# Performance work log

Measured on AMD Instinct MI355X. Metric: run time of the kernel, lower is better.

Reference implementation:

```python
import jax, jax.numpy as jnp
import numpy as np

DIM = 128
N_HEADS = 4
HEAD_DIM = DIM // N_HEADS  # 32
RANK = 8
SCALING = 16.0 / RANK      # alpha / rank = 2.0
ROPE_BASE = 10000.0
INV_SQRT_HD = 1.0 / float(np.sqrt(HEAD_DIM))


def _rope(x, cos, sin):
    # x: [B, S, H, D]; interleaved-pair rotation matching torch view(..., -1, 2)
    B, S, H, D = x.shape
    xr = x.reshape(B, S, H, D // 2, 2)
    x1, x2 = xr[..., 0], xr[..., 1]
    c = cos[None, :, None, :]  # [1, S, 1, D/2]
    s = sin[None, :, None, :]
    out = jnp.stack([x1 * c - x2 * s, x1 * s + x2 * c], axis=-1)
    return out.reshape(B, S, H, D)


def setup_inputs() -> dict:
    key = jax.random.key(0)
    ks = jax.random.split(key, 11)
    B, S = 128, 256
    w = lambda k, shp: jax.random.normal(k, shp, dtype=jnp.float32) * 0.05
    return {
        "x": jax.random.normal(ks[0], (B, S, DIM), dtype=jnp.float32),
        "wq": w(ks[1], (DIM, DIM)),
        "wk": w(ks[2], (DIM, DIM)),
        "wv": w(ks[3], (DIM, DIM)),
        "wo": w(ks[4], (DIM, DIM)),
        "lora_A_q": w(ks[5], (RANK, DIM)),
        "lora_B_q": w(ks[6], (DIM, RANK)),
        "lora_A_k": w(ks[7], (RANK, DIM)),
        "lora_B_k": w(ks[8], (DIM, RANK)),
        "lora_A_v": w(ks[9], (RANK, DIM)),
        "lora_B_v": w(ks[10], (DIM, RANK)),
    }


def reference(x, wq, wk, wv, wo, lora_A_q, lora_B_q, lora_A_k, lora_B_k,
              lora_A_v, lora_B_v):
    B, S, _ = x.shape
    # RoPE tables (HEAD_DIM split into pairs)
    pos = jnp.arange(S, dtype=jnp.float32)
    inv_freq = 1.0 / (ROPE_BASE ** (jnp.arange(0, HEAD_DIM, 2, dtype=jnp.float32) / HEAD_DIM))
    freqs = pos[:, None] * inv_freq[None, :]  # [S, HEAD_DIM/2]
    cos, sin = jnp.cos(freqs), jnp.sin(freqs)

    def proj(w, A, Bm):
        # base linear (no bias) + LoRA low-rank delta (dropout = eval identity)
        return x @ w.T + (x @ A.T @ Bm.T) * SCALING

    q = proj(wq, lora_A_q, lora_B_q).reshape(B, S, N_HEADS, HEAD_DIM)
    k = proj(wk, lora_A_k, lora_B_k).reshape(B, S, N_HEADS, HEAD_DIM)
    v = proj(wv, lora_A_v, lora_B_v).reshape(B, S, N_HEADS, HEAD_DIM)

    q = _rope(q, cos, sin).transpose(0, 2, 1, 3)  # [B, H, S, D]
    k = _rope(k, cos, sin).transpose(0, 2, 1, 3)
    v = v.transpose(0, 2, 1, 3)

    scores = jnp.einsum('bhqd,bhkd->bhqk', q, k) * INV_SQRT_HD
    causal = jnp.triu(jnp.ones((S, S), dtype=bool), k=1)
    scores = jnp.where(causal[None, None], -jnp.inf, scores)
    attn = jax.nn.softmax(scores, axis=-1)

    out = jnp.einsum('bhqk,bhkd->bhqd', attn, v)
    out = out.transpose(0, 2, 1, 3).reshape(B, S, DIM)
    return out @ wo.T
```

## Files before the change

### kernel.cpp

```cpp
#include <hip/hip_runtime.h>
#include <math.h>

typedef __attribute__((ext_vector_type(8))) short short8;
typedef __attribute__((ext_vector_type(4))) float floatx4;

#define NH 4
#define HD 32
#define DIM 128
#define SEQ 256
#define BATCH 128
#define BS (BATCH*SEQ)
#define RANK 8
#define SCALING 2.0f
#define INV_SQRT_HD 0.17677669529663687f
#define LOG2E 1.4426950408889634f

#if __has_builtin(__builtin_amdgcn_exp2f)
#define EXP2F __builtin_amdgcn_exp2f
#else
#define EXP2F exp2f
#endif

#define QB_OFF  (0ull)
#define KB_OFF  (8ull<<20)
#define VT_OFF  (16ull<<20)
#define XB_OFF  (24ull<<20)
#define WE_OFF  (32ull<<20)
#define TAB_OFF (33ull<<20)

static __device__ __forceinline__ unsigned short f2bf(float f) {
    unsigned u = __float_as_uint(f);
    return (unsigned short)((u + 0x7FFFu + ((u >> 16) & 1u)) >> 16);
}
static __device__ __forceinline__ unsigned packbf(float lo, float hi) {
    unsigned ua = __float_as_uint(lo), ub = __float_as_uint(hi);
    ua += 0x7FFFu + ((ua >> 16) & 1u);
    ub += 0x7FFFu + ((ub >> 16) & 1u);
    return __builtin_amdgcn_perm(ub, ua, 0x07060302);
}

__global__ __launch_bounds__(256) void prep_kernel(
    const float* __restrict__ x,
    const float* __restrict__ wq, const float* __restrict__ wk,
    const float* __restrict__ wv, const float* __restrict__ wo,
    const float* __restrict__ Aq, const float* __restrict__ Bq,
    const float* __restrict__ Ak, const float* __restrict__ Bk,
    const float* __restrict__ Av, const float* __restrict__ Bv,
    unsigned short* __restrict__ weffL, float* __restrict__ tab,
    unsigned short* __restrict__ xbL)
{
    const int bid = blockIdx.x, tid = threadIdx.x;
    if (bid < 32) {
        int t = bid * 256 + tid;
        int m    = t >> 11;
        int kc   = (t >> 9) & 3;
        int s    = (t >> 6) & 7;
        int lane = t & 63;
        int m16 = lane & 15, quad = lane >> 4;
        int row = (m < 3) ? ((s >> 1) * 32 + 2 * m16 + (s & 1)) : (s * 16 + m16);
        int col0 = kc * 32 + quad * 8;
        const float* W = m == 0 ? wq : (m == 1 ? wk : (m == 2 ? wv : wo));
        const float* A  = m == 0 ? Aq : (m == 1 ? Ak : Av);
        const float* Bm = m == 0 ? Bq : (m == 1 ? Bk : Bv);
        union { uint4 u4; unsigned short us[8]; } frag;
#pragma unroll
        for (int j = 0; j < 8; j++) {
            float val = W[row * DIM + col0 + j];
            if (m < 3) {
                float sacc = 0.f;
#pragma unroll
                for (int r = 0; r < RANK; r++)
                    sacc += Bm[row * RANK + r] * A[r * DIM + col0 + j];
                val += SCALING * sacc;
            }
            if (m == 0) val *= INV_SQRT_HD * LOG2E;
            frag.us[j] = f2bf(val);
        }
        *(uint4*)(weffL + (size_t)t * 8) = frag.u4;
    } else if (bid < 48) {
        int gid = (bid - 32) * 256 + tid;
        int spos = gid >> 4, i = gid & 15;
        float invf = exp2f(-0.83048202f * (float)i);
        float ang = (float)spos * invf;
        float c, s;
        sincosf(ang, &s, &c);
        tab[gid * 2]     = c;
        tab[gid * 2 + 1] = s;
    } else {
        int t = (bid - 48) * 256 + tid;
        int g    = t >> 8;
        int kc   = (t >> 6) & 3;
        int lane = t & 63;
        int m16 = lane & 15, quad = lane >> 4;
        const float* xp = x + (size_t)(g * 16 + m16) * DIM + kc * 32 + quad * 8;
        float4 f0 = *(const float4*)xp;
        float4 f1 = *(const float4*)(xp + 4);
        uint4 o;
        o.x = packbf(f0.x, f0.y); o.y = packbf(f0.z, f0.w);
        o.z = packbf(f1.x, f1.y); o.w = packbf(f1.z, f1.w);
        *(uint4*)(xbL + (size_t)t * 8) = o;
    }
}

#define VSTU 68
__global__ __launch_bounds__(256) void qkv_kernel(
    const unsigned short* __restrict__ xbL, const unsigned short* __restrict__ weffL,
    const float* __restrict__ tab,
    unsigned* __restrict__ qb, unsigned* __restrict__ kb,
    unsigned short* __restrict__ vtL)
{
    __shared__ unsigned vs_u[64 * VSTU];

    const int which = blockIdx.y;
    const unsigned short* W = weffL + which * DIM * DIM;

    const int tid = threadIdx.x;
    const int w = __builtin_amdgcn_readfirstlane(tid >> 6);
    const int lane = tid & 63;
    const int m16 = lane & 15, quad = lane >> 4;
    const int g = blockIdx.x * 4 + w;
    const int b = g >> 4;

    short8 afrag[4];
#pragma unroll
    for (int kc = 0; kc < 4; kc++)
        afrag[kc] = *(const short8*)(xbL + ((size_t)(g * 4 + kc) * 64 + lane) * 8);

    floatx4 acc_e[NH], acc_o[NH];
#pragma unroll
    for (int h = 0; h < NH; h++) {
        acc_e[h] = (floatx4){0.f, 0.f, 0.f, 0.f};
        acc_o[h] = (floatx4){0.f, 0.f, 0.f, 0.f};
    }

#pragma unroll
    for (int kc = 0; kc < 4; kc++) {
#pragma unroll
        for (int h = 0; h < NH; h++) {
            const unsigned short* base = W + ((kc * 8 + h * 2) * 64 + lane) * 8;
            short8 be = *(const short8*)base;
            short8 bo = *(const short8*)(base + 512);
            acc_e[h] = __builtin_amdgcn_mfma_f32_16x16x32_bf16(afrag[kc], be, acc_e[h], 0, 0, 0);
            acc_o[h] = __builtin_amdgcn_mfma_f32_16x16x32_bf16(afrag[kc], bo, acc_o[h], 0, 0, 0);
        }
    }

    if (which < 2) {
        unsigned* outp = which == 0 ? qb : kb;
        const int sposq = (g & 15) * 16 + quad * 4;
#pragma unroll
        for (int r = 0; r < 4; r++) {
            int spos = sposq + r;
            float2 cs = *(const float2*)(tab + ((size_t)spos * 16 + m16) * 2);
#pragma unroll
            for (int h = 0; h < NH; h++) {
                float e = acc_e[h][r], o = acc_o[h][r];
                outp[((size_t)(b * NH + h) * SEQ + spos) * (HD / 2) + m16] =
                    packbf(e * cs.x - o * cs.y, e * cs.y + o * cs.x);
            }
        }
    } else {
        const int cloc = w >> 1;
        const int sig0 = (w & 1);
#pragma unroll
        for (int r = 0; r < 4; r++) {
            int sig = 8 * quad + 2 * r + sig0;
            int col = cloc * 32 + (sig ^ ((m16 & 3) << 3));
#pragma unroll
            for (int h = 0; h < NH; h++)
                vs_u[(h * 16 + m16) * VSTU + col] = packbf(acc_e[h][r], acc_o[h][r]);
        }
        __syncthreads();
        const int cb = ((blockIdx.x * 64) & 255) >> 5;
        const size_t bhbase = (size_t)(b * NH) * 8;
#pragma unroll
        for (int it = 0; it < 4; it++) {
            int f = it * 256 + tid;
            int c_l = f >> 9;
            int h   = (f >> 7) & 3;
            int p   = (f >> 6) & 1;
            int ln  = f & 63;
            int fm16 = ln & 15, fq = ln >> 4;
            const unsigned* src = vs_u + (h * 16 + fm16) * VSTU + c_l * 32
                                + ((fq ^ (fm16 & 3)) * 8);
            uint4 a = *(const uint4*)src;
            uint4 bb = *(const uint4*)(src + 4);
            unsigned sel = p ? 0x07060302u : 0x05040100u;
            uint4 o;
            o.x = __builtin_amdgcn_perm(a.y,  a.x,  sel);
            o.y = __builtin_amdgcn_perm(a.w,  a.z,  sel);
            o.z = __builtin_amdgcn_perm(bb.y, bb.x, sel);
            o.w = __builtin_amdgcn_perm(bb.w, bb.z, sel);
            *(uint4*)(vtL + (((bhbase + h * 8 + cb + c_l) * 2 + p) * 512 + ln * 8)) = o;
        }
    }
}

#define PBU 20
#define OS_STRIDE 136
__global__ __launch_bounds__(256) void attn_kernel(
    const unsigned short* __restrict__ qbs, const unsigned short* __restrict__ kbs,
    const unsigned short* __restrict__ vtL, const unsigned short* __restrict__ woL,
    float* __restrict__ out)
{
    __shared__ unsigned pbuf_u[4 * 2 * 16 * PBU];
    __shared__ unsigned short os[32 * OS_STRIDE];

    const int qt = blockIdx.x;
    const int b  = blockIdx.y;
    const int q0 = qt * 32;
    const int tid = threadIdx.x;
    const int w = __builtin_amdgcn_readfirstlane(tid >> 6);
    const int lane = tid & 63;
    const int m16 = lane & 15, quad = lane >> 4;

    const size_t bh = (size_t)(b * NH + w);
    const unsigned short* qrow = qbs + (bh * SEQ + q0) * HD;
    const unsigned short* krow = kbs + bh * SEQ * HD;
    const unsigned short* vbase = vtL + bh * 8 * 1024;

    short8 aq[2];
#pragma unroll
    for (int qs = 0; qs < 2; qs++)
        aq[qs] = *(const short8*)(qrow + (size_t)(qs * 16 + m16) * HD + quad * 8);

    const short ob = (short)0x3F80;
    const short8 bones = {ob, ob, ob, ob, ob, ob, ob, ob};

    floatx4 o_e[2], o_o[2], o_l[2];
#pragma unroll
    for (int qs = 0; qs < 2; qs++) {
        o_e[qs] = (floatx4){0.f, 0.f, 0.f, 0.f};
        o_o[qs] = (floatx4){0.f, 0.f, 0.f, 0.f};
        o_l[qs] = (floatx4){0.f, 0.f, 0.f, 0.f};
    }

    const floatx4 z4 = (floatx4){0.f, 0.f, 0.f, 0.f};
    const int nchunks = qt + 1;

    short8 cbk0, cbk1, cbve, cbvo, nbk0, nbk1, nbve, nbvo;
    {
        cbk0 = *(const short8*)(krow + (size_t)m16 * HD + quad * 8);
        cbk1 = *(const short8*)(krow + (size_t)(16 + m16) * HD + quad * 8);
        const unsigned short* vp = vbase + lane * 8;
        cbve = *(const short8*)vp;
        cbvo = *(const short8*)(vp + 512);
    }

    unsigned* pw = pbuf_u + (w * 2) * 16 * PBU;

    for (int c = 0; c < nchunks; c++) {
        const int cn = (c + 1 < nchunks) ? c + 1 : c;
        {
            const unsigned short* kp = krow + (size_t)cn * 32 * HD;
            nbk0 = *(const short8*)(kp + (size_t)m16 * HD + quad * 8);
            nbk1 = *(const short8*)(kp + (size_t)(16 + m16) * HD + quad * 8);
            const unsigned short* vp = vbase + (size_t)cn * 1024 + lane * 8;
            nbve = *(const short8*)vp;
            nbvo = *(const short8*)(vp + 512);
        }
        const int k0 = c * 32;
        const int kg0 = k0 + m16, kg1 = k0 + 16 + m16;
#pragma unroll
        for (int qs = 0; qs < 2; qs++) {
            floatx4 s0 = __builtin_amdgcn_mfma_f32_16x16x32_bf16(aq[qs], cbk0, z4, 0, 0, 0);
            floatx4 s1 = __builtin_amdgcn_mfma_f32_16x16x32_bf16(aq[qs], cbk1, z4, 0, 0, 0);
            unsigned* pq = pw + qs * 16 * PBU;
            const int qg = q0 + qs * 16 + quad * 4;
#pragma unroll
            for (int r = 0; r < 4; r++) {
                float p0 = (kg0 <= qg + r) ? EXP2F(s0[r]) : 0.f;
                float p1 = (kg1 <= qg + r) ? EXP2F(s1[r]) : 0.f;
                pq[(quad * 4 + r) * PBU + m16] = packbf(p0, p1);
            }
            const unsigned short* pqs = (const unsigned short*)pq;
            short8 ap = *(const short8*)(pqs + m16 * (PBU * 2) + quad * 8);
            o_e[qs] = __builtin_amdgcn_mfma_f32_16x16x32_bf16(ap, cbve, o_e[qs], 0, 0, 0);
            o_o[qs] = __builtin_amdgcn_mfma_f32_16x16x32_bf16(ap, cbvo, o_o[qs], 0, 0, 0);
            o_l[qs] = __builtin_amdgcn_mfma_f32_16x16x32_bf16(ap, bones, o_l[qs], 0, 0, 0);
        }
        cbk0 = nbk0; cbk1 = nbk1; cbve = nbve; cbvo = nbvo;
    }

    unsigned* osu = (unsigned*)os;
#pragma unroll
    for (int qs = 0; qs < 2; qs++)
#pragma unroll
        for (int r = 0; r < 4; r++) {
            float inv = 1.f / o_l[qs][r];
            osu[(qs * 16 + quad * 4 + r) * (OS_STRIDE / 2) + w * 16 + m16] =
                packbf(o_e[qs][r] * inv, o_o[qs][r] * inv);
        }
    __syncthreads();

    const int tw = (w & 1) * 16;
    const int dbase = (w >> 1) * 64;

    short8 af[4];
#pragma unroll
    for (int kc = 0; kc < 4; kc++)
        af[kc] = *(const short8*)(os + (tw + m16) * OS_STRIDE + kc * 32 + quad * 8);

    floatx4 acc[4];
#pragma unroll
    for (int nt = 0; nt < 4; nt++) acc[nt] = (floatx4){0.f, 0.f, 0.f, 0.f};
#pragma unroll
    for (int kc = 0; kc < 4; kc++)
#pragma unroll
        for (int nt = 0; nt < 4; nt++) {
            short8 bf = *(const short8*)(woL + ((kc * 8 + (w >> 1) * 4 + nt) * 64 + lane) * 8);
            acc[nt] = __builtin_amdgcn_mfma_f32_16x16x32_bf16(af[kc], bf, acc[nt], 0, 0, 0);
        }

#pragma unroll
    for (int nt = 0; nt < 4; nt++)
#pragma unroll
        for (int r = 0; r < 4; r++)
            out[(size_t)(b * SEQ + q0 + tw + quad * 4 + r) * DIM
                + dbase + nt * 16 + m16] = acc[nt][r];
}

extern "C" void kernel_launch(void* const* d_in, const int* in_sizes, int n_in,
                              void* d_out, int out_size, void* d_ws, size_t ws_size,
                              hipStream_t stream)
{
    const float* x  = (const float*)d_in[0];
    const float* wq = (const float*)d_in[1];
    const float* wk = (const float*)d_in[2];
    const float* wv = (const float*)d_in[3];
    const float* wo = (const float*)d_in[4];
    const float* Aq = (const float*)d_in[5];
    const float* Bq = (const float*)d_in[6];
    const float* Ak = (const float*)d_in[7];
    const float* Bk = (const float*)d_in[8];
    const float* Av = (const float*)d_in[9];
    const float* Bv = (const float*)d_in[10];
    float* out = (float*)d_out;
    char* ws = (char*)d_ws;

    unsigned*       qb    = (unsigned*)(ws + QB_OFF);
    unsigned*       kb    = (unsigned*)(ws + KB_OFF);
    unsigned short* vtL   = (unsigned short*)(ws + VT_OFF);
    unsigned short* xbL   = (unsigned short*)(ws + XB_OFF);
    unsigned short* weffL = (unsigned short*)(ws + WE_OFF);
    float*          tab   = (float*)(ws + TAB_OFF);

    prep_kernel<<<48 + 2048, 256, 0, stream>>>(
        x, wq, wk, wv, wo, Aq, Bq, Ak, Bk, Av, Bv, weffL, tab, xbL);
    qkv_kernel<<<dim3(BS / 64, 3), 256, 0, stream>>>(xbL, weffL, tab, qb, kb, vtL);
    attn_kernel<<<dim3(8, BATCH), 256, 0, stream>>>(
        (const unsigned short*)qb, (const unsigned short*)kb, vtL,
        weffL + 3 * DIM * DIM, out);
}
```

Baseline: 127.7 us.

## Fuse QKV projection, attention and output projection into one per-batch kernel

Replaces the separate qkv and attention kernels with a single 512-thread kernel per batch element. Q, K and V are computed on the fly and kept in LDS, so they never round-trip through global memory. K/V chunks of 64 positions are produced and consumed in a staged loop, with each wave owning 32 query rows. The grid shrinks to only 128 blocks, which leaves many of the device's CUs idle. The causal work is also unbalanced across waves, with later waves doing more chunks while earlier waves wait at barriers.

Result: slower. 164.6 us (+28.9%).

```diff
diff --git a/kernel.cpp b/kernel.cpp
--- a/kernel.cpp
+++ b/kernel.cpp
@@ -21,12 +21,9 @@
 #define EXP2F exp2f
 #endif
 
-#define QB_OFF  (0ull)
-#define KB_OFF  (8ull<<20)
-#define VT_OFF  (16ull<<20)
-#define XB_OFF  (24ull<<20)
-#define WE_OFF  (32ull<<20)
-#define TAB_OFF (33ull<<20)
+#define XB_OFF  (0ull)
+#define WE_OFF  (9ull<<20)
+#define TAB_OFF (10ull<<20)
 
 static __device__ __forceinline__ unsigned short f2bf(float f) {
     unsigned u = __float_as_uint(f);
@@ -102,222 +99,213 @@
     }
 }
 
+#define KSTS 40
 #define VSTU 68
-__global__ __launch_bounds__(256) void qkv_kernel(
-    const unsigned short* __restrict__ xbL, const unsigned short* __restrict__ weffL,
+#define QOSU 68
+#define PBU  20
+
+#define LDS_KS   (4*64*KSTS*2)
+#define LDS_VS   (64*VSTU*4)
+#define LDS_PB   (8*16*PBU*4)
+
+__global__ __launch_bounds__(512, 2) void mega_kernel(
+    const unsigned short* __restrict__ xbL,
+    const unsigned short* __restrict__ weffL,
     const float* __restrict__ tab,
-    unsigned* __restrict__ qb, unsigned* __restrict__ kb,
-    unsigned short* __restrict__ vtL)
+    float* __restrict__ out)
 {
-    __shared__ unsigned vs_u[64 * VSTU];
-
-    const int which = blockIdx.y;
-    const unsigned short* W = weffL + which * DIM * DIM;
-
+    __shared__ __align__(16) char lds[LDS_KS + LDS_VS + LDS_PB];
+    unsigned short* ks  = (unsigned short*)lds;
+    unsigned*       ksu = (unsigned*)lds;
+    unsigned*       vs  = (unsigned*)(lds + LDS_KS);
+    unsigned*       pb  = (unsigned*)(lds + LDS_KS + LDS_VS);
+    unsigned*       qo  = (unsigned*)lds;
+
+    const int b = blockIdx.x;
     const int tid = threadIdx.x;
     const int w = __builtin_amdgcn_readfirstlane(tid >> 6);
     const int lane = tid & 63;
     const int m16 = lane & 15, quad = lane >> 4;
-    const int g = blockIdx.x * 4 + w;
-    const int b = g >> 4;
-
-    short8 afrag[4];
-#pragma unroll
-    for (int kc = 0; kc < 4; kc++)
-        afrag[kc] = *(const short8*)(xbL + ((size_t)(g * 4 + kc) * 64 + lane) * 8);
-
-    floatx4 acc_e[NH], acc_o[NH];
-#pragma unroll
-    for (int h = 0; h < NH; h++) {
-        acc_e[h] = (floatx4){0.f, 0.f, 0.f, 0.f};
-        acc_o[h] = (floatx4){0.f, 0.f, 0.f, 0.f};
+
+    const short ob = (short)0x3F80;
+    const short8 bones = {ob, ob, ob, ob, ob, ob, ob, ob};
+    const floatx4 z4 = (floatx4){0.f, 0.f, 0.f, 0.f};
+
+    unsigned* qrow_w = qo + (size_t)w * 16 * QOSU;
+
+    short8 aq[2][NH];
+#pragma unroll
+    for (int qs = 0; qs < 2; qs++) {
+        const int g = b * 16 + w * 2 + qs;
+        short8 xf[4];
+#pragma unroll
+        for (int kc = 0; kc < 4; kc++)
+            xf[kc] = *(const short8*)(xbL + ((size_t)(g * 4 + kc) * 64 + lane) * 8);
+        floatx4 ae[NH], ao[NH];
+#pragma unroll
+        for (int h = 0; h < NH; h++) { ae[h] = z4; ao[h] = z4; }
+#pragma unroll
+        for (int kc = 0; kc < 4; kc++)
+#pragma unroll
+            for (int h = 0; h < NH; h++) {
+                const unsigned short* bp = weffL + ((size_t)(kc * 8 + h * 2) * 64 + lane) * 8;
+                short8 be = *(const short8*)bp;
+                short8 bo = *(const short8*)(bp + 512);
+                ae[h] = __builtin_amdgcn_mfma_f32_16x16x32_bf16(xf[kc], be, ae[h], 0, 0, 0);
+                ao[h] = __builtin_amdgcn_mfma_f32_16x16x32_bf16(xf[kc], bo, ao[h], 0, 0, 0);
+            }
+        const int sbase = w * 32 + qs * 16 + quad * 4;
+#pragma unroll
+        for (int r = 0; r < 4; r++) {
+            float2 cs = *(const float2*)(tab + ((size_t)(sbase + r) * 16 + m16) * 2);
+#pragma unroll
+            for (int h = 0; h < NH; h++) {
+                float e = ae[h][r], o = ao[h][r];
+                qrow_w[(quad * 4 + r) * QOSU + h * 16 + m16] =
+                    packbf(e * cs.x - o * cs.y, e * cs.y + o * cs.x);
+            }
+        }
+#pragma unroll
+        for (int h = 0; h < NH; h++)
+            aq[qs][h] = *(const short8*)((const unsigned short*)qo
+                        + ((size_t)(w * 16 + m16) * QOSU) * 2 + h * 32 + quad * 8);
     }
-
-#pragma unroll
-    for (int kc = 0; kc < 4; kc++) {
-#pragma unroll
-        for (int h = 0; h < NH; h++) {
-            const unsigned short* base = W + ((kc * 8 + h * 2) * 64 + lane) * 8;
-            short8 be = *(const short8*)base;
-            short8 bo = *(const short8*)(base + 512);
-            acc_e[h] = __builtin_amdgcn_mfma_f32_16x16x32_bf16(afrag[kc], be, acc_e[h], 0, 0, 0);
-            acc_o[h] = __builtin_amdgcn_mfma_f32_16x16x32_bf16(afrag[kc], bo, acc_o[h], 0, 0, 0);
-        }
-    }
-
-    if (which < 2) {
-        unsigned* outp = which == 0 ? qb : kb;
-        const int sposq = (g & 15) * 16 + quad * 4;
-#pragma unroll
-        for (int r = 0; r < 4; r++) {
-            int spos = sposq + r;
-            float2 cs = *(const float2*)(tab + ((size_t)spos * 16 + m16) * 2);
-#pragma unroll
-            for (int h = 0; h < NH; h++) {
-                float e = acc_e[h][r], o = acc_o[h][r];
-                outp[((size_t)(b * NH + h) * SEQ + spos) * (HD / 2) + m16] =
-                    packbf(e * cs.x - o * cs.y, e * cs.y + o * cs.x);
-            }
-        }
-    } else {
-        const int cloc = w >> 1;
-        const int sig0 = (w & 1);
-#pragma unroll
-        for (int r = 0; r < 4; r++) {
-            int sig = 8 * quad + 2 * r + sig0;
-            int col = cloc * 32 + (sig ^ ((m16 & 3) << 3));
-#pragma unroll
-            for (int h = 0; h < NH; h++)
-                vs_u[(h * 16 + m16) * VSTU + col] = packbf(acc_e[h][r], acc_o[h][r]);
+    __syncthreads();
+
+    floatx4 oe[2][NH], oo[2][NH], ol[2][NH];
+#pragma unroll
+    for (int qs = 0; qs < 2; qs++)
+#pragma unroll
+        for (int h = 0; h < NH; h++) { oe[qs][h] = z4; oo[qs][h] = z4; ol[qs][h] = z4; }
+
+    const int role_v = w >> 2;
+    const int sub = w & 3;
+
+    for (int c = 0; c < 4; c++) {
+        {
+            const int g = b * 16 + c * 4 + sub;
+            short8 xf[4];
+#pragma unroll
+            for (int kc = 0; kc < 4; kc++)
+                xf[kc] = *(const short8*)(xbL + ((size_t)(g * 4 + kc) * 64 + lane) * 8);
+            const unsigned short* Wm = weffL + (size_t)(role_v ? 2 : 1) * DIM * DIM;
+            floatx4 ae[NH], ao[NH];
+#pragma unroll
+            for (int h = 0; h < NH; h++) { ae[h] = z4; ao[h] = z4; }
+#pragma unroll
+            for (int kc = 0; kc < 4; kc++)
+#pragma unroll
+                for (int h = 0; h < NH; h++) {
+                    const unsigned short* bp = Wm + ((size_t)(kc * 8 + h * 2) * 64 + lane) * 8;
+                    short8 be = *(const short8*)bp;
+                    short8 bo = *(const short8*)(bp + 512);
+                    ae[h] = __builtin_amdgcn_mfma_f32_16x16x32_bf16(xf[kc], be, ae[h], 0, 0, 0);
+                    ao[h] = __builtin_amdgcn_mfma_f32_16x16x32_bf16(xf[kc], bo, ao[h], 0, 0, 0);
+                }
+            if (!role_v) {
+                const int sbase = c * 64 + sub * 16 + quad * 4;
+#pragma unroll
+                for (int r = 0; r < 4; r++) {
+                    float2 cs = *(const float2*)(tab + ((size_t)(sbase + r) * 16 + m16) * 2);
+#pragma unroll
+                    for (int h = 0; h < NH; h++) {
+                        float e = ae[h][r], o = ao[h][r];
+                        ksu[(size_t)(h * 64 + sub * 16 + quad * 4 + r) * (KSTS / 2) + m16] =
+                            packbf(e * cs.x - o * cs.y, e * cs.y + o * cs.x);
+                    }
+                }
+            } else {
+                const int t16 = sub & 1, s32 = sub >> 1;
+#pragma unroll
+                for (int r = 0; r < 4; r++) {
+                    int kap = 8 * quad + 2 * r + t16;
+                    int col = s32 * 32 + (kap ^ ((m16 & 3) << 3));
+#pragma unroll
+                    for (int h = 0; h < NH; h++)
+                        vs[(size_t)(h * 16 + m16) * VSTU + col] = packbf(ae[h][r], ao[h][r]);
+                }
+            }
         }
         __syncthreads();
-        const int cb = ((blockIdx.x * 64) & 255) >> 5;
-        const size_t bhbase = (size_t)(b * NH) * 8;
-#pragma unroll
-        for (int it = 0; it < 4; it++) {
-            int f = it * 256 + tid;
-            int c_l = f >> 9;
-            int h   = (f >> 7) & 3;
-            int p   = (f >> 6) & 1;
-            int ln  = f & 63;
-            int fm16 = ln & 15, fq = ln >> 4;
-            const unsigned* src = vs_u + (h * 16 + fm16) * VSTU + c_l * 32
-                                + ((fq ^ (fm16 & 3)) * 8);
-            uint4 a = *(const uint4*)src;
-            uint4 bb = *(const uint4*)(src + 4);
-            unsigned sel = p ? 0x07060302u : 0x05040100u;
-            uint4 o;
-            o.x = __builtin_amdgcn_perm(a.y,  a.x,  sel);
-            o.y = __builtin_amdgcn_perm(a.w,  a.z,  sel);
-            o.z = __builtin_amdgcn_perm(bb.y, bb.x, sel);
-            o.w = __builtin_amdgcn_perm(bb.w, bb.z, sel);
-            *(uint4*)(vtL + (((bhbase + h * 8 + cb + c_l) * 2 + p) * 512 + ln * 8)) = o;
+        if (w >= 2 * c) {
+            const int smax = (w - 2 * c >= 1) ? 2 : 1;
+            unsigned* pw = pb + (size_t)w * 16 * PBU;
+            for (int s32 = 0; s32 < smax; s32++) {
+                const int k0 = c * 64 + s32 * 32;
+#pragma unroll
+                for (int h = 0; h < NH; h++) {
+                    const unsigned short* kp = ks + (size_t)(h * 64 + s32 * 32) * KSTS;
+                    short8 kb0 = *(const short8*)(kp + (size_t)m16 * KSTS + quad * 8);
+                    short8 kb1 = *(const short8*)(kp + (size_t)(16 + m16) * KSTS + quad * 8);
+                    const unsigned* vp = vs + (size_t)(h * 16 + m16) * VSTU + s32 * 32
+                                       + ((quad ^ (m16 & 3)) * 8);
+                    uint4 va = *(const uint4*)vp;
+                    uint4 vb = *(const uint4*)(vp + 4);
+                    union { short8 v; unsigned u[4]; } fe, fo;
+                    fe.u[0] = __builtin_amdgcn_perm(va.y, va.x, 0x05040100u);
+                    fe.u[1] = __builtin_amdgcn_perm(va.w, va.z, 0x05040100u);
+                    fe.u[2] = __builtin_amdgcn_perm(vb.y, vb.x, 0x05040100u);
+                    fe.u[3] = __builtin_amdgcn_perm(vb.w, vb.z, 0x05040100u);
+                    fo.u[0] = __builtin_amdgcn_perm(va.y, va.x, 0x07060302u);
+                    fo.u[1] = __builtin_amdgcn_perm(va.w, va.z, 0x07060302u);
+                    fo.u[2] = __builtin_amdgcn_perm(vb.y, vb.x, 0x07060302u);
+                    fo.u[3] = __builtin_amdgcn_perm(vb.w, vb.z, 0x07060302u);
+#pragma unroll
+                    for (int qs = 0; qs < 2; qs++) {
+                        floatx4 s0 = __builtin_amdgcn_mfma_f32_16x16x32_bf16(aq[qs][h], kb0, z4, 0, 0, 0);
+                        floatx4 s1 = __builtin_amdgcn_mfma_f32_16x16x32_bf16(aq[qs][h], kb1, z4, 0, 0, 0);
+                        const int qg = w * 32 + qs * 16 + quad * 4;
+#pragma unroll
+                        for (int r = 0; r < 4; r++) {
+                            float p0 = (k0 + m16      <= qg + r) ? EXP2F(s0[r]) : 0.f;
+                            float p1 = (k0 + 16 + m16 <= qg + r) ? EXP2F(s1[r]) : 0.f;
+                            pw[(quad * 4 + r) * PBU + m16] = packbf(p0, p1);
+                        }
+                        short8 ap = *(const short8*)((const unsigned short*)pw
+                                    + m16 * (PBU * 2) + quad * 8);
+                        oe[qs][h] = __builtin_amdgcn_mfma_f32_16x16x32_bf16(ap, fe.v, oe[qs][h], 0, 0, 0);
+                        oo[qs][h] = __builtin_amdgcn_mfma_f32_16x16x32_bf16(ap, fo.v, oo[qs][h], 0, 0, 0);
+                        ol[qs][h] = __builtin_amdgcn_mfma_f32_16x16x32_bf16(ap, bones, ol[qs][h], 0, 0, 0);
+                    }
+                }
+            }
         }
+        __syncthreads();
     }
-}
-
-#define PBU 20
-#define OS_STRIDE 136
-__global__ __launch_bounds__(256) void attn_kernel(
-    const unsigned short* __restrict__ qbs, const unsigned short* __restrict__ kbs,
-    const unsigned short* __restrict__ vtL, const unsigned short* __restrict__ woL,
-    float* __restrict__ out)
-{
-    __shared__ unsigned pbuf_u[4 * 2 * 16 * PBU];
-    __shared__ unsigned short os[32 * OS_STRIDE];
-
-    const int qt = blockIdx.x;
-    const int b  = blockIdx.y;
-    const int q0 = qt * 32;
-    const int tid = threadIdx.x;
-    const int w = __builtin_amdgcn_readfirstlane(tid >> 6);
-    const int lane = tid & 63;
-    const int m16 = lane & 15, quad = lane >> 4;
-
-    const size_t bh = (size_t)(b * NH + w);
-    const unsigned short* qrow = qbs + (bh * SEQ + q0) * HD;
-    const unsigned short* krow = kbs + bh * SEQ * HD;
-    const unsigned short* vbase = vtL + bh * 8 * 1024;
-
-    short8 aq[2];
-#pragma unroll
-    for (int qs = 0; qs < 2; qs++)
-        aq[qs] = *(const short8*)(qrow + (size_t)(qs * 16 + m16) * HD + quad * 8);
-
-    const short ob = (short)0x3F80;
-    const short8 bones = {ob, ob, ob, ob, ob, ob, ob, ob};
-
-    floatx4 o_e[2], o_o[2], o_l[2];
+
+    const unsigned short* Wo = weffL + (size_t)3 * DIM * DIM;
 #pragma unroll
     for (int qs = 0; qs < 2; qs++) {
-        o_e[qs] = (floatx4){0.f, 0.f, 0.f, 0.f};
-        o_o[qs] = (floatx4){0.f, 0.f, 0.f, 0.f};
-        o_l[qs] = (floatx4){0.f, 0.f, 0.f, 0.f};
+#pragma unroll
+        for (int r = 0; r < 4; r++)
+#pragma unroll
+            for (int h = 0; h < NH; h++) {
+                float inv = 1.f / ol[qs][h][r];
+                qrow_w[(quad * 4 + r) * QOSU + h * 16 + m16] =
+                    packbf(oe[qs][h][r] * inv, oo[qs][h][r] * inv);
+            }
+        short8 af[4];
+#pragma unroll
+        for (int kc = 0; kc < 4; kc++)
+            af[kc] = *(const short8*)((const unsigned short*)qo
+                     + ((size_t)(w * 16 + m16) * QOSU) * 2 + kc * 32 + quad * 8);
+        floatx4 acc[8];
+#pragma unroll
+        for (int nt = 0; nt < 8; nt++) acc[nt] = z4;
+#pragma unroll
+        for (int kc = 0; kc < 4; kc++)
+#pragma unroll
+            for (int nt = 0; nt < 8; nt++) {
+                short8 bf = *(const short8*)(Wo + ((size_t)(kc * 8 + nt) * 64 + lane) * 8);
+                acc[nt] = __builtin_amdgcn_mfma_f32_16x16x32_bf16(af[kc], bf, acc[nt], 0, 0, 0);
+            }
+#pragma unroll
+        for (int nt = 0; nt < 8; nt++)
+#pragma unroll
+            for (int r = 0; r < 4; r++)
+                out[(size_t)(b * SEQ + w * 32 + qs * 16 + quad * 4 + r) * DIM
+                    + nt * 16 + m16] = acc[nt][r];
     }
-
-    const floatx4 z4 = (floatx4){0.f, 0.f, 0.f, 0.f};
-    const int nchunks = qt + 1;
-
-    short8 cbk0, cbk1, cbve, cbvo, nbk0, nbk1, nbve, nbvo;
-    {
-        cbk0 = *(const short8*)(krow + (size_t)m16 * HD + quad * 8);
-        cbk1 = *(const short8*)(krow + (size_t)(16 + m16) * HD + quad * 8);
-        const unsigned short* vp = vbase + lane * 8;
-        cbve = *(const short8*)vp;
-        cbvo = *(const short8*)(vp + 512);
-    }
-
-    unsigned* pw = pbuf_u + (w * 2) * 16 * PBU;
-
-    for (int c = 0; c < nchunks; c++) {
-        const int cn = (c + 1 < nchunks) ? c + 1 : c;
-        {
-            const unsigned short* kp = krow + (size_t)cn * 32 * HD;
-            nbk0 = *(const short8*)(kp + (size_t)m16 * HD + quad * 8);
-            nbk1 = *(const short8*)(kp + (size_t)(16 + m16) * HD + quad * 8);
-            const unsigned short* vp = vbase + (size_t)cn * 1024 + lane * 8;
-            nbve = *(const short8*)vp;
-            nbvo = *(const short8*)(vp + 512);
-        }
-        const int k0 = c * 32;
-        const int kg0 = k0 + m16, kg1 = k0 + 16 + m16;
-#pragma unroll
-        for (int qs = 0; qs < 2; qs++) {
-            floatx4 s0 = __builtin_amdgcn_mfma_f32_16x16x32_bf16(aq[qs], cbk0, z4, 0, 0, 0);
-            floatx4 s1 = __builtin_amdgcn_mfma_f32_16x16x32_bf16(aq[qs], cbk1, z4, 0, 0, 0);
-            unsigned* pq = pw + qs * 16 * PBU;
-            const int qg = q0 + qs * 16 + quad * 4;
-#pragma unroll
-            for (int r = 0; r < 4; r++) {
-                float p0 = (kg0 <= qg + r) ? EXP2F(s0[r]) : 0.f;
-                float p1 = (kg1 <= qg + r) ? EXP2F(s1[r]) : 0.f;
-                pq[(quad * 4 + r) * PBU + m16] = packbf(p0, p1);
-            }
-            const unsigned short* pqs = (const unsigned short*)pq;
-            short8 ap = *(const short8*)(pqs + m16 * (PBU * 2) + quad * 8);
-            o_e[qs] = __builtin_amdgcn_mfma_f32_16x16x32_bf16(ap, cbve, o_e[qs], 0, 0, 0);
-            o_o[qs] = __builtin_amdgcn_mfma_f32_16x16x32_bf16(ap, cbvo, o_o[qs], 0, 0, 0);
-            o_l[qs] = __builtin_amdgcn_mfma_f32_16x16x32_bf16(ap, bones, o_l[qs], 0, 0, 0);
-        }
-        cbk0 = nbk0; cbk1 = nbk1; cbve = nbve; cbvo = nbvo;
-    }
-
-    unsigned* osu = (unsigned*)os;
-#pragma unroll
-    for (int qs = 0; qs < 2; qs++)
-#pragma unroll
-        for (int r = 0; r < 4; r++) {
-            float inv = 1.f / o_l[qs][r];
-            osu[(qs * 16 + quad * 4 + r) * (OS_STRIDE / 2) + w * 16 + m16] =
-                packbf(o_e[qs][r] * inv, o_o[qs][r] * inv);
-        }
-    __syncthreads();
-
-    const int tw = (w & 1) * 16;
-    const int dbase = (w >> 1) * 64;
-
-    short8 af[4];
-#pragma unroll
-    for (int kc = 0; kc < 4; kc++)
-        af[kc] = *(const short8*)(os + (tw + m16) * OS_STRIDE + kc * 32 + quad * 8);
-
-    floatx4 acc[4];
-#pragma unroll
-    for (int nt = 0; nt < 4; nt++) acc[nt] = (floatx4){0.f, 0.f, 0.f, 0.f};
-#pragma unroll
-    for (int kc = 0; kc < 4; kc++)
-#pragma unroll
-        for (int nt = 0; nt < 4; nt++) {
-            short8 bf = *(const short8*)(woL + ((kc * 8 + (w >> 1) * 4 + nt) * 64 + lane) * 8);
-            acc[nt] = __builtin_amdgcn_mfma_f32_16x16x32_bf16(af[kc], bf, acc[nt], 0, 0, 0);
-        }
-
-#pragma unroll
-    for (int nt = 0; nt < 4; nt++)
-#pragma unroll
-        for (int r = 0; r < 4; r++)
-            out[(size_t)(b * SEQ + q0 + tw + quad * 4 + r) * DIM
-                + dbase + nt * 16 + m16] = acc[nt][r];
 }
 
 extern "C" void kernel_launch(void* const* d_in, const int* in_sizes, int n_in,
@@ -338,17 +326,11 @@
     float* out = (float*)d_out;
     char* ws = (char*)d_ws;
 
-    unsigned*       qb    = (unsigned*)(ws + QB_OFF);
-    unsigned*       kb    = (unsigned*)(ws + KB_OFF);
-    unsigned short* vtL   = (unsigned short*)(ws + VT_OFF);
     unsigned short* xbL   = (unsigned short*)(ws + XB_OFF);
     unsigned short* weffL = (unsigned short*)(ws + WE_OFF);
     float*          tab   = (float*)(ws + TAB_OFF);
 
     prep_kernel<<<48 + 2048, 256, 0, stream>>>(
         x, wq, wk, wv, wo, Aq, Bq, Ak, Bk, Av, Bv, weffL, tab, xbL);
-    qkv_kernel<<<dim3(BS / 64, 3), 256, 0, stream>>>(xbL, weffL, tab, qb, kb, vtL);
-    attn_kernel<<<dim3(8, BATCH), 256, 0, stream>>>(
-        (const unsigned short*)qb, (const unsigned short*)kb, vtL,
-        weffL + 3 * DIM * DIM, out);
-}
+    mega_kernel<<<BATCH, 512, 0, stream>>>(xbL, weffL, tab, out);
+}
```

## Pair causal query tiles per attention block and spread weight prep across more threads

Applied to the files above, without the earlier changes.

The attention kernel now launches half as many blocks, and each block handles two query tiles (7-p and p). This gives every block the same total number of causal key chunks and removes load imbalance from the triangular mask. The weight-merge part of the prep kernel now uses four times as many threads, each producing two bf16 values instead of eight, which shortens the serial per-thread LoRA work. In exchange, each attention block runs longer and serialises two tiles, with an extra barrier between them, and the grid drops to 512 blocks.

After: 118.2 us, median of 2. 1.08x faster.

```diff
diff --git a/kernel.cpp b/kernel.cpp
--- a/kernel.cpp
+++ b/kernel.cpp
@@ -50,35 +50,35 @@
     unsigned short* __restrict__ xbL)
 {
     const int bid = blockIdx.x, tid = threadIdx.x;
-    if (bid < 32) {
+    if (bid < 128) {
         int t = bid * 256 + tid;
-        int m    = t >> 11;
-        int kc   = (t >> 9) & 3;
-        int s    = (t >> 6) & 7;
-        int lane = t & 63;
+        int m    = t >> 13;
+        int kc   = (t >> 11) & 3;
+        int s    = (t >> 8) & 7;
+        int lane = (t >> 2) & 63;
+        int e    = t & 3;
         int m16 = lane & 15, quad = lane >> 4;
         int row = (m < 3) ? ((s >> 1) * 32 + 2 * m16 + (s & 1)) : (s * 16 + m16);
-        int col0 = kc * 32 + quad * 8;
+        int col = kc * 32 + quad * 8 + 2 * e;
         const float* W = m == 0 ? wq : (m == 1 ? wk : (m == 2 ? wv : wo));
         const float* A  = m == 0 ? Aq : (m == 1 ? Ak : Av);
         const float* Bm = m == 0 ? Bq : (m == 1 ? Bk : Bv);
-        union { uint4 u4; unsigned short us[8]; } frag;
-#pragma unroll
-        for (int j = 0; j < 8; j++) {
-            float val = W[row * DIM + col0 + j];
-            if (m < 3) {
-                float sacc = 0.f;
-#pragma unroll
-                for (int r = 0; r < RANK; r++)
-                    sacc += Bm[row * RANK + r] * A[r * DIM + col0 + j];
-                val += SCALING * sacc;
-            }
-            if (m == 0) val *= INV_SQRT_HD * LOG2E;
-            frag.us[j] = f2bf(val);
-        }
-        *(uint4*)(weffL + (size_t)t * 8) = frag.u4;
-    } else if (bid < 48) {
-        int gid = (bid - 32) * 256 + tid;
+        float v0 = W[row * DIM + col], v1 = W[row * DIM + col + 1];
+        if (m < 3) {
+            float s0 = 0.f, s1 = 0.f;
+#pragma unroll
+            for (int r = 0; r < RANK; r++) {
+                float br = Bm[row * RANK + r];
+                s0 += br * A[r * DIM + col];
+                s1 += br * A[r * DIM + col + 1];
+            }
+            v0 += SCALING * s0;
+            v1 += SCALING * s1;
+        }
+        if (m == 0) { v0 *= INV_SQRT_HD * LOG2E; v1 *= INV_SQRT_HD * LOG2E; }
+        ((unsigned*)weffL)[t] = packbf(v0, v1);
+    } else if (bid < 144) {
+        int gid = (bid - 128) * 256 + tid;
         int spos = gid >> 4, i = gid & 15;
         float invf = exp2f(-0.83048202f * (float)i);
         float ang = (float)spos * invf;
@@ -87,7 +87,7 @@
         tab[gid * 2]     = c;
         tab[gid * 2 + 1] = s;
     } else {
-        int t = (bid - 48) * 256 + tid;
+        int t = (bid - 144) * 256 + tid;
         int g    = t >> 8;
         int kc   = (t >> 6) & 3;
         int lane = t & 63;
@@ -206,118 +206,117 @@
     __shared__ unsigned pbuf_u[4 * 2 * 16 * PBU];
     __shared__ unsigned short os[32 * OS_STRIDE];
 
-    const int qt = blockIdx.x;
+    const int p  = blockIdx.x;
     const int b  = blockIdx.y;
-    const int q0 = qt * 32;
     const int tid = threadIdx.x;
     const int w = __builtin_amdgcn_readfirstlane(tid >> 6);
     const int lane = tid & 63;
     const int m16 = lane & 15, quad = lane >> 4;
 
     const size_t bh = (size_t)(b * NH + w);
-    const unsigned short* qrow = qbs + (bh * SEQ + q0) * HD;
     const unsigned short* krow = kbs + bh * SEQ * HD;
     const unsigned short* vbase = vtL + bh * 8 * 1024;
 
-    short8 aq[2];
-#pragma unroll
-    for (int qs = 0; qs < 2; qs++)
-        aq[qs] = *(const short8*)(qrow + (size_t)(qs * 16 + m16) * HD + quad * 8);
-
     const short ob = (short)0x3F80;
     const short8 bones = {ob, ob, ob, ob, ob, ob, ob, ob};
-
-    floatx4 o_e[2], o_o[2], o_l[2];
-#pragma unroll
-    for (int qs = 0; qs < 2; qs++) {
-        o_e[qs] = (floatx4){0.f, 0.f, 0.f, 0.f};
-        o_o[qs] = (floatx4){0.f, 0.f, 0.f, 0.f};
-        o_l[qs] = (floatx4){0.f, 0.f, 0.f, 0.f};
-    }
-
     const floatx4 z4 = (floatx4){0.f, 0.f, 0.f, 0.f};
-    const int nchunks = qt + 1;
-
-    short8 cbk0, cbk1, cbve, cbvo, nbk0, nbk1, nbve, nbvo;
-    {
-        cbk0 = *(const short8*)(krow + (size_t)m16 * HD + quad * 8);
-        cbk1 = *(const short8*)(krow + (size_t)(16 + m16) * HD + quad * 8);
-        const unsigned short* vp = vbase + lane * 8;
-        cbve = *(const short8*)vp;
-        cbvo = *(const short8*)(vp + 512);
-    }
-
     unsigned* pw = pbuf_u + (w * 2) * 16 * PBU;
 
-    for (int c = 0; c < nchunks; c++) {
-        const int cn = (c + 1 < nchunks) ? c + 1 : c;
+    for (int half = 0; half < 2; half++) {
+        const int qt = half ? p : (7 - p);
+        const int q0 = qt * 32;
+        const unsigned short* qrow = qbs + (bh * SEQ + q0) * HD;
+
+        short8 aq[2];
+#pragma unroll
+        for (int qs = 0; qs < 2; qs++)
+            aq[qs] = *(const short8*)(qrow + (size_t)(qs * 16 + m16) * HD + quad * 8);
+
+        floatx4 o_e[2], o_o[2], o_l[2];
+#pragma unroll
+        for (int qs = 0; qs < 2; qs++) { o_e[qs] = z4; o_o[qs] = z4; o_l[qs] = z4; }
+
+        const int nchunks = qt + 1;
+        short8 cbk0, cbk1, cbve, cbvo, nbk0, nbk1, nbve, nbvo;
         {
-            const unsigned short* kp = krow + (size_t)cn * 32 * HD;
-            nbk0 = *(const short8*)(kp + (size_t)m16 * HD + quad * 8);
-            nbk1 = *(const short8*)(kp + (size_t)(16 + m16) * HD + quad * 8);
-            const unsigned short* vp = vbase + (size_t)cn * 1024 + lane * 8;
-            nbve = *(const short8*)vp;
-            nbvo = *(const short8*)(vp + 512);
-        }
-        const int k0 = c * 32;
-        const int kg0 = k0 + m16, kg1 = k0 + 16 + m16;
-#pragma unroll
-        for (int qs = 0; qs < 2; qs++) {
-            floatx4 s0 = __builtin_amdgcn_mfma_f32_16x16x32_bf16(aq[qs], cbk0, z4, 0, 0, 0);
-            floatx4 s1 = __builtin_amdgcn_mfma_f32_16x16x32_bf16(aq[qs], cbk1, z4, 0, 0, 0);
-            unsigned* pq = pw + qs * 16 * PBU;
-            const int qg = q0 + qs * 16 + quad * 4;
+            cbk0 = *(const short8*)(krow + (size_t)m16 * HD + quad * 8);
+            cbk1 = *(const short8*)(krow + (size_t)(16 + m16) * HD + quad * 8);
+            const unsigned short* vp = vbase + lane * 8;
+            cbve = *(const short8*)vp;
+            cbvo = *(const short8*)(vp + 512);
+        }
+
+        for (int c = 0; c < nchunks; c++) {
+            const int cn = (c + 1 < nchunks) ? c + 1 : c;
+            {
+                const unsigned short* kp = krow + (size_t)cn * 32 * HD;
+                nbk0 = *(const short8*)(kp + (size_t)m16 * HD + quad * 8);
+                nbk1 = *(const short8*)(kp + (size_t)(16 + m16) * HD + quad * 8);
+                const unsigned short* vp = vbase + (size_t)cn * 1024 + lane * 8;
+                nbve = *(const short8*)vp;
+                nbvo = *(const short8*)(vp + 512);
+            }
+            const int k0 = c * 32;
+            const int kg0 = k0 + m16, kg1 = k0 + 16 + m16;
+#pragma unroll
+            for (int qs = 0; qs < 2; qs++) {
+                floatx4 s0 = __builtin_amdgcn_mfma_f32_16x16x32_bf16(aq[qs], cbk0, z4, 0, 0, 0);
+                floatx4 s1 = __builtin_amdgcn_mfma_f32_16x16x32_bf16(aq[qs], cbk1, z4, 0, 0, 0);
+                unsigned* pq = pw + qs * 16 * PBU;
+                const int qg = q0 + qs * 16 + quad * 4;
+#pragma unroll
+                for (int r = 0; r < 4; r++) {
+                    float p0 = (kg0 <= qg + r) ? EXP2F(s0[r]) : 0.f;
+                    float p1 = (kg1 <= qg + r) ? EXP2F(s1[r]) : 0.f;
+                    pq[(quad * 4 + r) * PBU + m16] = packbf(p0, p1);
+                }
+                const unsigned short* pqs = (const unsigned short*)pq;
+                short8 ap = *(const short8*)(pqs + m16 * (PBU * 2) + quad * 8);
+                o_e[qs] = __builtin_amdgcn_mfma_f32_16x16x32_bf16(ap, cbve, o_e[qs], 0, 0, 0);
+                o_o[qs] = __builtin_amdgcn_mfma_f32_16x16x32_bf16(ap, cbvo, o_o[qs], 0, 0, 0);
+                o_l[qs] = __builtin_amdgcn_mfma_f32_16x16x32_bf16(ap, bones, o_l[qs], 0, 0, 0);
+            }
+            cbk0 = nbk0; cbk1 = nbk1; cbve = nbve; cbvo = nbvo;
+        }
+
+        if (half) __syncthreads();
+        unsigned* osu = (unsigned*)os;
+#pragma unroll
+        for (int qs = 0; qs < 2; qs++)
 #pragma unroll
             for (int r = 0; r < 4; r++) {
-                float p0 = (kg0 <= qg + r) ? EXP2F(s0[r]) : 0.f;
-                float p1 = (kg1 <= qg + r) ? EXP2F(s1[r]) : 0.f;
-                pq[(quad * 4 + r) * PBU + m16] = packbf(p0, p1);
-            }
-            const unsigned short* pqs = (const unsigned short*)pq;
-            short8 ap = *(const short8*)(pqs + m16 * (PBU * 2) + quad * 8);
-            o_e[qs] = __builtin_amdgcn_mfma_f32_16x16x32_bf16(ap, cbve, o_e[qs], 0, 0, 0);
-            o_o[qs] = __builtin_amdgcn_mfma_f32_16x16x32_bf16(ap, cbvo, o_o[qs], 0, 0, 0);
-            o_l[qs] = __builtin_amdgcn_mfma_f32_16x16x32_bf16(ap, bones, o_l[qs], 0, 0, 0);
-        }
-        cbk0 = nbk0; cbk1 = nbk1; cbve = nbve; cbvo = nbvo;
-    }
-
-    unsigned* osu = (unsigned*)os;
-#pragma unroll
-    for (int qs = 0; qs < 2; qs++)
-#pragma unroll
-        for (int r = 0; r < 4; r++) {
-            float inv = 1.f / o_l[qs][r];
-            osu[(qs * 16 + quad * 4 + r) * (OS_STRIDE / 2) + w * 16 + m16] =
-                packbf(o_e[qs][r] * inv, o_o[qs][r] * inv);
-        }
-    __syncthreads();
-
-    const int tw = (w & 1) * 16;
-    const int dbase = (w >> 1) * 64;
-
-    short8 af[4];
-#pragma unroll
-    for (int kc = 0; kc < 4; kc++)
-        af[kc] = *(const short8*)(os + (tw + m16) * OS_STRIDE + kc * 32 + quad * 8);
-
-    floatx4 acc[4];
-#pragma unroll
-    for (int nt = 0; nt < 4; nt++) acc[nt] = (floatx4){0.f, 0.f, 0.f, 0.f};
-#pragma unroll
-    for (int kc = 0; kc < 4; kc++)
-#pragma unroll
-        for (int nt = 0; nt < 4; nt++) {
-            short8 bf = *(const short8*)(woL + ((kc * 8 + (w >> 1) * 4 + nt) * 64 + lane) * 8);
-            acc[nt] = __builtin_amdgcn_mfma_f32_16x16x32_bf16(af[kc], bf, acc[nt], 0, 0, 0);
-        }
-
-#pragma unroll
-    for (int nt = 0; nt < 4; nt++)
-#pragma unroll
-        for (int r = 0; r < 4; r++)
-            out[(size_t)(b * SEQ + q0 + tw + quad * 4 + r) * DIM
-                + dbase + nt * 16 + m16] = acc[nt][r];
+                float inv = 1.f / o_l[qs][r];
+                osu[(qs * 16 + quad * 4 + r) * (OS_STRIDE / 2) + w * 16 + m16] =
+                    packbf(o_e[qs][r] * inv, o_o[qs][r] * inv);
+            }
+        __syncthreads();
+
+        const int tw = (w & 1) * 16;
+        const int dbase = (w >> 1) * 64;
+
+        short8 af[4];
+#pragma unroll
+        for (int kc = 0; kc < 4; kc++)
+            af[kc] = *(const short8*)(os + (tw + m16) * OS_STRIDE + kc * 32 + quad * 8);
+
+        floatx4 acc[4];
+#pragma unroll
+        for (int nt = 0; nt < 4; nt++) acc[nt] = z4;
+#pragma unroll
+        for (int kc = 0; kc < 4; kc++)
+#pragma unroll
+            for (int nt = 0; nt < 4; nt++) {
+                short8 bf = *(const short8*)(woL + ((kc * 8 + (w >> 1) * 4 + nt) * 64 + lane) * 8);
+                acc[nt] = __builtin_amdgcn_mfma_f32_16x16x32_bf16(af[kc], bf, acc[nt], 0, 0, 0);
+            }
+
+#pragma unroll
+        for (int nt = 0; nt < 4; nt++)
+#pragma unroll
+            for (int r = 0; r < 4; r++)
+                out[(size_t)(b * SEQ + q0 + tw + quad * 4 + r) * DIM
+                    + dbase + nt * 16 + m16] = acc[nt][r];
+    }
 }
 
 extern "C" void kernel_launch(void* const* d_in, const int* in_sizes, int n_in,
@@ -345,10 +344,10 @@
     unsigned short* weffL = (unsigned short*)(ws + WE_OFF);
     float*          tab   = (float*)(ws + TAB_OFF);
 
-    prep_kernel<<<48 + 2048, 256, 0, stream>>>(
+    prep_kernel<<<144 + 2048, 256, 0, stream>>>(
         x, wq, wk, wv, wo, Aq, Bq, Ak, Bk, Av, Bv, weffL, tab, xbL);
     qkv_kernel<<<dim3(BS / 64, 3), 256, 0, stream>>>(xbL, weffL, tab, qb, kb, vtL);
-    attn_kernel<<<dim3(8, BATCH), 256, 0, stream>>>(
+    attn_kernel<<<dim3(4, BATCH), 256, 0, stream>>>(
         (const unsigned short*)qb, (const unsigned short*)kb, vtL,
         weffL + 3 * DIM * DIM, out);
 }
```
